# Optimization experiments

Hardware: AMD Instinct MI355X
Metric: run time of the kernel (lower is better)

Reference implementation:

```python
import jax, jax.numpy as jnp
import numpy as np

N_NET = 4000000   # length of concatenated model output values
R = 1000000       # number of rotated sp blocks (s0=9, s1=3)
NG = 1024         # number of geometries in the single bsize group
B = 64            # basis size (orbitals per molecule)
NE = 7            # number of elements for Eref
EREP = 2000000    # repulsive pair terms
ROT_LEN = 2 + R * 9


def setup_inputs() -> dict:
    key = jax.random.key(0)
    ks = jax.random.split(key, 14)
    net_vals = jax.random.normal(ks[0], (N_NET,), jnp.float32)
    rot_tensors = jax.random.normal(ks[1], (R, 9, 3), jnp.float32)
    S = jax.random.normal(ks[2], (NG, B, B), jnp.float32)
    S = 0.5 * (S + jnp.swapaxes(S, -2, -1))  # overlap is symmetric
    G = jax.random.normal(ks[3], (NG, B, B), jnp.float32)
    G = 0.5 * (G + jnp.swapaxes(G, -2, -1))  # gamma matrix is symmetric
    rho = jax.random.normal(ks[4], (NG, B, B), jnp.float32)
    qneutral = jax.random.uniform(ks[5], (NG, B, 1), dtype=jnp.float32)
    occ_rho_mask = (jax.random.uniform(ks[6], (NG, B, B)) > 0.5).astype(jnp.float32)
    phiS = 0.1 * jax.random.normal(ks[7], (NG, B, B), jnp.float32)
    zcounts = jax.random.uniform(ks[8], (1, NE), dtype=jnp.float32)
    ref_vars = jax.random.normal(ks[9], (NE,), jnp.float32)
    gather_rot = jax.random.randint(ks[10], (R * 3,), 0, N_NET)
    gather_oper = jax.random.randint(ks[11], (NG * B * B,), 0, ROT_LEN)
    gather_rep = jax.random.randint(ks[12], (EREP,), 0, N_NET)
    segsum_rep = jnp.sort(jax.random.randint(ks[13], (EREP,), 0, NG))
    return dict(net_vals=net_vals, rot_tensors=rot_tensors, S=S, G=G, rho=rho,
                qneutral=qneutral, occ_rho_mask=occ_rho_mask, phiS=phiS,
                zcounts=zcounts, ref_vars=ref_vars, gather_rot=gather_rot,
                gather_oper=gather_oper, gather_rep=gather_rep, segsum_rep=segsum_rep)


def reference(net_vals, rot_tensors, S, G, rho, qneutral, occ_rho_mask, phiS,
              zcounts, ref_vars, gather_rot, gather_oper, gather_rep, segsum_rep):
    ng, b, _ = S.shape
    # --- rotation stage: gather net_vals, batched small matmul [R,9,3]@[R,3,1]
    rot_vals = net_vals[gather_rot].reshape(-1, 3)[:, :, None]          # [R,3,1]
    rot = jnp.matmul(rot_tensors, rot_vals)[:, :, 0]                    # [R,9]
    rot_out = jnp.concatenate([jnp.array([0.0, 1.0], S.dtype), rot.reshape(-1)])
    # --- operator gather: build H blocks per geometry
    H = rot_out[gather_oper].reshape(ng, b, b)
    # --- charge fluctuations and coulomb matrix
    qbasis = rho * S
    dQ = qneutral - jnp.sum(qbasis, axis=2, keepdims=True)              # [ng,b,1]
    ep = jnp.matmul(G, dQ)                                              # [ng,b,1]
    couMat = -0.5 * S * (ep + jnp.swapaxes(ep, -2, -1))
    F = H + couMat
    # --- repulsive energy: gather + segment-sum over geometries
    Erep = jax.ops.segment_sum(net_vals[gather_rep], segsum_rep, num_segments=ng)
    # --- generalized eigenproblem via provided phiS (S^{-1/2})
    fockp = jnp.swapaxes(phiS, -2, -1) @ (F @ phiS)
    eorb, C = jnp.linalg.eigh(fockp)
    orb = phiS @ C
    orb_filled = occ_rho_mask * orb
    rho_out = 2.0 * (orb_filled @ jnp.swapaxes(orb_filled, -2, -1))
    # --- electronic energy
    ener1 = jnp.sum(rho_out * H, axis=(1, 2))
    ener2 = 0.5 * jnp.squeeze(jnp.swapaxes(dQ, -2, -1) @ (G @ dQ), axis=(1, 2))
    Eelec = ener1 + ener2
    Eref = jnp.dot(zcounts[0], ref_vars)
    return (H, dQ, Erep, eorb, rho_out, Eelec, Eref)
```

## Files before the change

### kernel.cpp

```cpp
#include <hip/hip_runtime.h>

typedef unsigned int uint_t;

#define NGc     1024
#define Bc      64
#define LDA     67
#define LDV     66
#define Rc      1000000
#define NNETc   4000000
#define EREPc   2000000
#define ROTLENc 9000002

#define OFF_H     0
#define OFF_DQ    4194304
#define OFF_EREP  4259840
#define OFF_EORB  4260864
#define OFF_RHO   4326400
#define OFF_EELEC 8520704
#define OFF_EREF  8521728

__global__ void k_rot(const float* __restrict__ rot_t,
                      const int*   __restrict__ gather_rot,
                      const float* __restrict__ net_vals,
                      float*       __restrict__ ws)
{
    int r = blockIdx.x * 256 + threadIdx.x;
    if (r >= Rc) return;
    const int* gr = gather_rot + (size_t)r * 3;
    int i0 = gr[0], i1 = gr[1], i2 = gr[2];
    i0 = ((unsigned)i0 < (unsigned)NNETc) ? i0 : 0;
    i1 = ((unsigned)i1 < (unsigned)NNETc) ? i1 : 0;
    i2 = ((unsigned)i2 < (unsigned)NNETc) ? i2 : 0;
    float v0 = net_vals[i0], v1 = net_vals[i1], v2 = net_vals[i2];
    const float* tt = rot_t + (size_t)r * 27;
    float* wp = ws + (size_t)r * 9;
    #pragma unroll
    for (int c = 0; c < 9; c++)
        wp[c] = tt[c*3+0] * v0 + tt[c*3+1] * v1 + tt[c*3+2] * v2;
}

__global__ void k_hgather4(const int*   __restrict__ idx,
                           const float* __restrict__ ws,
                           float*       __restrict__ out)
{
    int t4 = blockIdx.x * 256 + threadIdx.x;
    const int4 id4 = ((const int4*)idx)[t4];
    float4 hv;
    {
        int id = id4.x;
        hv.x = (id >= 2 && id < ROTLENc) ? ws[id - 2] : ((id == 1) ? 1.0f : 0.0f);
    }
    {
        int id = id4.y;
        hv.y = (id >= 2 && id < ROTLENc) ? ws[id - 2] : ((id == 1) ? 1.0f : 0.0f);
    }
    {
        int id = id4.z;
        hv.z = (id >= 2 && id < ROTLENc) ? ws[id - 2] : ((id == 1) ? 1.0f : 0.0f);
    }
    {
        int id = id4.w;
        hv.w = (id >= 2 && id < ROTLENc) ? ws[id - 2] : ((id == 1) ? 1.0f : 0.0f);
    }
    ((float4*)(out + OFF_H))[t4] = hv;
}

__global__ void k_hgather(const int*   __restrict__ idx,
                          const float* __restrict__ rot_t,
                          const int*   __restrict__ gather_rot,
                          const float* __restrict__ net_vals,
                          float*       __restrict__ out)
{
    int t = blockIdx.x * 256 + threadIdx.x;
    if (t >= NGc * Bc * Bc) return;
    int id = idx[t];
    float hv;
    if (id >= 2 && id < ROTLENc) {
        int k = id - 2;
        int r = k / 9;
        int c = k - r * 9;
        const float* tt = rot_t + (size_t)r * 27 + (size_t)c * 3;
        const int*   gr = gather_rot + (size_t)r * 3;
        int i0 = gr[0], i1 = gr[1], i2 = gr[2];
        i0 = ((unsigned)i0 < (unsigned)NNETc) ? i0 : 0;
        i1 = ((unsigned)i1 < (unsigned)NNETc) ? i1 : 0;
        i2 = ((unsigned)i2 < (unsigned)NNETc) ? i2 : 0;
        hv = tt[0] * net_vals[i0] + tt[1] * net_vals[i1] + tt[2] * net_vals[i2];
    } else {
        hv = (id == 1) ? 1.0f : 0.0f;
    }
    out[OFF_H + t] = hv;
}

__global__ void k_erep_seg(const float* __restrict__ net_vals,
                           const int*   __restrict__ gather_rep,
                           const int*   __restrict__ segsum,
                           const float* __restrict__ zcounts,
                           const float* __restrict__ ref_vars,
                           float*       __restrict__ out)
{
    __shared__ int   sB[2];
    __shared__ float red[256];
    const int g = blockIdx.x, tid = threadIdx.x;

    if (tid < 2) {
        int target = g + tid;
        int lo = 0, hi = EREPc;
        while (lo < hi) {
            int mid = (lo + hi) >> 1;
            if (segsum[mid] < target) lo = mid + 1; else hi = mid;
        }
        sB[tid] = lo;
    }
    __syncthreads();
    const int s = sB[0], e = sB[1];
    float acc = 0.f;
    for (int i = s + tid; i < e; i += 256) {
        int gi = gather_rep[i];
        gi = ((unsigned)gi < (unsigned)NNETc) ? gi : 0;
        acc += net_vals[gi];
    }
    red[tid] = acc;
    __syncthreads();
    for (int sN = 128; sN > 0; sN >>= 1) {
        if (tid < sN) red[tid] += red[tid + sN];
        __syncthreads();
    }
    if (tid == 0) out[OFF_EREP + g] = red[0];

    if (g == 0 && tid == 0) {
        float er = 0.f;
        for (int j = 0; j < 7; j++) er += zcounts[j] * ref_vars[j];
        out[OFF_EREF] = er;
    }
}

__global__ __launch_bounds__(256, 4) void k_geom(
    const float* __restrict__ Sg_,  const float* __restrict__ Gg_,
    const float* __restrict__ rho_, const float* __restrict__ qn_,
    const float* __restrict__ mask_,const float* __restrict__ phiS_,
    float* out)
{
    __shared__ float Ab[Bc * LDA];
    __shared__ float Vb[Bc * LDV];
    __shared__ float dqs[Bc];
    __shared__ float epv[Bc];
    __shared__ float red[256];
    __shared__ float diagA[Bc];
    __shared__ int   perm[Bc];
    __shared__ float2 csCS[32];
    __shared__ float sOffArr[4];

    const int g    = blockIdx.x;
    const int tid  = threadIdx.x;
    const size_t gb = (size_t)g * 4096;

    const float* Sp = Sg_  + gb;
    const float* Gp = Gg_  + gb;
    const float* Rp = rho_ + gb;
    const float* Mp = mask_+ gb;
    const float* Pp = phiS_+ gb;
    const float4* P4 = (const float4*)Pp;
    const float* Hp = out + OFF_H + gb;

    #pragma unroll
    for (int m = 0; m < 16; m++) {
        int e = tid + m * 256;
        int i = e >> 6, j = e & 63;
        Vb[i*LDV + j] = Sp[e];
    }
    __syncthreads();

    {
        int i = tid >> 2, qr = tid & 3;
        float acc = 0.f;
        #pragma unroll
        for (int jj = 0; jj < 16; jj++) {
            int j = qr * 16 + jj;
            acc += Rp[i * 64 + j] * Vb[i*LDV + j];
        }
        acc += __shfl_xor(acc, 1, 64);
        acc += __shfl_xor(acc, 2, 64);
        if (qr == 0) dqs[i] = qn_[(size_t)g * 64 + i] - acc;
    }
    #pragma unroll
    for (int m = 0; m < 16; m++) {
        int e = tid + m * 256;
        int i = e >> 6, j = e & 63;
        Ab[i*LDA + j] = Gp[e];
    }
    __syncthreads();
    {
        int i = tid >> 2, qr = tid & 3;
        float acc = 0.f;
        #pragma unroll
        for (int jj = 0; jj < 16; jj++) {
            int j = qr * 16 + jj;
            acc += Ab[i*LDA + j] * dqs[j];
        }
        acc += __shfl_xor(acc, 1, 64);
        acc += __shfl_xor(acc, 2, 64);
        if (qr == 0) epv[i] = acc;
    }
    __syncthreads();
    float ener2r = 0.f;
    if (tid < 64) {
        float v = dqs[tid] * epv[tid];
        #pragma unroll
        for (int o = 1; o < 64; o <<= 1) v += __shfl_xor(v, o, 64);
        if (tid == 0) ener2r = 0.5f * v;
    }
    #pragma unroll
    for (int m = 0; m < 16; m++) {
        int e = tid + m * 256;
        int i = e >> 6, j = e & 63;
        Ab[i*LDA + j] = Hp[e] - 0.5f * Vb[i*LDV + j] * (epv[i] + epv[j]);
    }
    __syncthreads();

    const int tx = tid & 15, ty = tid >> 4;
    const int row0 = ty * 4, col0 = tx * 4;
    float acc4[4][4];

    #pragma unroll
    for (int u = 0; u < 4; u++)
        #pragma unroll
        for (int v = 0; v < 4; v++) acc4[u][v] = 0.f;
    for (int k = 0; k < 64; k++) {
        float av[4];
        #pragma unroll
        for (int u = 0; u < 4; u++) av[u] = Ab[(row0 + u) * LDA + k];
        union { float4 v4; float f[4]; } b4;
        b4.v4 = P4[k * 16 + tx];
        #pragma unroll
        for (int u = 0; u < 4; u++)
            #pragma unroll
            for (int v = 0; v < 4; v++) acc4[u][v] += av[u] * b4.f[v];
    }
    #pragma unroll
    for (int u = 0; u < 4; u++)
        #pragma unroll
        for (int v = 0; v < 4; v++) Vb[(row0 + u) * LDV + col0 + v] = acc4[u][v];
    __syncthreads();

    #pragma unroll
    for (int u = 0; u < 4; u++)
        #pragma unroll
        for (int v = 0; v < 4; v++) acc4[u][v] = 0.f;
    for (int k = 0; k < 64; k++) {
        union { float4 v4; float f[4]; } a4;
        a4.v4 = P4[k * 16 + ty];
        float bv[4];
        #pragma unroll
        for (int v = 0; v < 4; v++) bv[v] = Vb[k * LDV + col0 + v];
        #pragma unroll
        for (int u = 0; u < 4; u++)
            #pragma unroll
            for (int v = 0; v < 4; v++) acc4[u][v] += a4.f[u] * bv[v];
    }
    {
        float fr = 0.f;
        #pragma unroll
        for (int u = 0; u < 4; u++)
            #pragma unroll
            for (int v = 0; v < 4; v++) {
                Ab[(row0 + u) * LDA + col0 + v] = acc4[u][v];
                fr += acc4[u][v] * acc4[u][v];
            }
        if (tx == ty) {
            #pragma unroll
            for (int u = 0; u < 4; u++) diagA[row0 + u] = acc4[u][u];
        }
        red[tid] = fr;
    }
    __syncthreads();
    for (int sN = 128; sN > 0; sN >>= 1) {
        if (tid < sN) red[tid] += red[tid + sN];
        __syncthreads();
    }
    const float anorm2 = red[0];

    #pragma unroll
    for (int m = 0; m < 17; m++) {
        int e = tid + m * 256;
        if (e < Bc * LDV) Vb[e] = 0.f;
    }
    __syncthreads();
    if (tid < 64) { Vb[tid * LDV + tid] = 1.f; perm[tid] = tid; }

    const float skip2 = anorm2 * 1e-18f;
    const float conv2 = anorm2 * 4e-14f;

    const int myi = tid & 31;
    const int jb  = tid >> 5;
    const int cb  = jb << 3;

    int iP, iQ, iPa, iQa, iPv, iQv;
    {
        iP = (myi == 0) ? 63 : myi;
        iQ = (myi == 0) ? 0  : 63 - myi;
        iPa = iP * LDA; iQa = iQ * LDA;
        iPv = iP * LDV; iQv = iQ * LDV;
    }
    int jP[4], jQ[4];
    #pragma unroll
    for (int k = 0; k < 4; k++) {
        int x = jb + (k << 3);
        jP[k] = (x == 0) ? 63 : x;
        jQ[k] = (x == 0) ? 0  : 63 - x;
    }
    const bool dgk[4] = { myi == jb, myi == jb + 8,
                          myi == jb + 16, myi == jb + 24 };

    for (int sweep = 0; sweep < 10; ++sweep) {
        float offacc = 0.f;
        for (int r = 0; r < 63; r++) {
            if (tid < 32) {
                float app = diagA[iP];
                float aqq = diagA[iQ];
                float apq = Ab[iPa + iQ];
                float a2 = apq * apq;
                offacc += a2;
                float c = 1.f, s = 0.f;
                if (a2 > skip2) {
                    float tau = (aqq - app) * __builtin_amdgcn_rcpf(apq + apq);
                    float tt = __builtin_amdgcn_rcpf(
                        fabsf(tau) + __builtin_amdgcn_sqrtf(1.f + tau * tau));
                    tt = (tau < 0.f) ? -tt : tt;
                    c = __builtin_amdgcn_rsqf(1.f + tt * tt);
                    s = tt * c;
                    diagA[iP] = app - tt * apq;
                    diagA[iQ] = aqq + tt * apq;
                    Ab[iPa + iQ] = 0.f;
                    Ab[iQa + iP] = 0.f;
                }
                csCS[myi] = make_float2(c, s);
            }
            __syncthreads();

            float2 me = csCS[myi];
            const float cO = me.x, sO = me.y;
            #pragma unroll
            for (int k = 0; k < 4; k++) {
                float2 cj = csCS[jb + (k << 3)];
                float cc = cj.x, ss = cj.y;
                if (!dgk[k] && (sO != 0.f || ss != 0.f)) {
                    int aPP = iPa + jP[k], aPQ = iPa + jQ[k];
                    int aQP = iQa + jP[k], aQQ = iQa + jQ[k];
                    float a = Ab[aPP], b = Ab[aPQ];
                    float d = Ab[aQP], e = Ab[aQQ];
                    float a1 = cc * a - ss * b, b1 = ss * a + cc * b;
                    float d1 = cc * d - ss * e, e1 = ss * d + cc * e;
                    Ab[aPP] = cO * a1 - sO * d1;
                    Ab[aQP] = sO * a1 + cO * d1;
                    Ab[aPQ] = cO * b1 - sO * e1;
                    Ab[aQQ] = sO * b1 + cO * e1;
                }
            }
            if (sO != 0.f) {
                float2* vp = (float2*)&Vb[iPv + cb];
                float2* vq = (float2*)&Vb[iQv + cb];
                #pragma unroll
                for (int e2 = 0; e2 < 4; e2++) {
                    float2 xp = vp[e2], xq = vq[e2];
                    float2 np, nq;
                    np.x = cO * xp.x - sO * xq.x;  np.y = cO * xp.y - sO * xq.y;
                    nq.x = sO * xp.x + cO * xq.x;  nq.y = sO * xp.y + cO * xq.y;
                    vp[e2] = np; vq[e2] = nq;
                }
            }
            {
                int nP  = (iP == 62) ? 0 : ((iP == 63) ? 63 : iP + 1);
                int nPa = (iP == 62) ? 0 : ((iP == 63) ? iPa : iPa + LDA);
                int nPv = (iP == 62) ? 0 : ((iP == 63) ? iPv : iPv + LDV);
                int nQ  = (iQ == 62) ? 0 : iQ + 1;
                int nQa = (iQ == 62) ? 0 : iQa + LDA;
                int nQv = (iQ == 62) ? 0 : iQv + LDV;
                iP = nP; iPa = nPa; iPv = nPv; iQ = nQ; iQa = nQa; iQv = nQv;
            }
            #pragma unroll
            for (int k = 0; k < 4; k++) {
                int p = jP[k], q = jQ[k];
                jP[k] = (p == 62) ? 0 : ((p == 63) ? 63 : p + 1);
                jQ[k] = (q == 62) ? 0 : q + 1;
            }
            __syncthreads();
        }
        float t2 = offacc;
        #pragma unroll
        for (int o = 1; o < 32; o <<= 1) t2 += __shfl_xor(t2, o, 64);
        if (tid == 0) sOffArr[0] = t2;
        __syncthreads();
        if (sOffArr[0] < conv2) break;
    }

    if (tid < 64) {
        float e = diagA[tid]; int rk = 0;
        for (int j = 0; j < 64; j++) {
            float ej = diagA[j];
            rk += (ej < e || (ej == e && j < tid)) ? 1 : 0;
        }
        rk &= 63;
        perm[rk] = tid;
        out[OFF_EORB + (size_t)g * 64 + rk] = e;
    }
    __syncthreads();

    {
        int pc0 = perm[col0 + 0] & 63, pc1 = perm[col0 + 1] & 63;
        int pc2 = perm[col0 + 2] & 63, pc3 = perm[col0 + 3] & 63;
        #pragma unroll
        for (int u = 0; u < 4; u++)
            #pragma unroll
            for (int v = 0; v < 4; v++) acc4[u][v] = 0.f;
        for (int kk = 0; kk < 16; kk++) {
            union { float4 v4; float f[4]; } a0, a1, a2u, a3;
            a0.v4  = P4[(row0 + 0) * 16 + kk];
            a1.v4  = P4[(row0 + 1) * 16 + kk];
            a2u.v4 = P4[(row0 + 2) * 16 + kk];
            a3.v4  = P4[(row0 + 3) * 16 + kk];
            #pragma unroll
            for (int t = 0; t < 4; t++) {
                int k = (kk << 2) + t;
                float b0 = Vb[pc0*LDV + k], b1 = Vb[pc1*LDV + k];
                float b2 = Vb[pc2*LDV + k], b3 = Vb[pc3*LDV + k];
                acc4[0][0] += a0.f[t]  * b0; acc4[0][1] += a0.f[t]  * b1;
                acc4[0][2] += a0.f[t]  * b2; acc4[0][3] += a0.f[t]  * b3;
                acc4[1][0] += a1.f[t]  * b0; acc4[1][1] += a1.f[t]  * b1;
                acc4[1][2] += a1.f[t]  * b2; acc4[1][3] += a1.f[t]  * b3;
                acc4[2][0] += a2u.f[t] * b0; acc4[2][1] += a2u.f[t] * b1;
                acc4[2][2] += a2u.f[t] * b2; acc4[2][3] += a2u.f[t] * b3;
                acc4[3][0] += a3.f[t]  * b0; acc4[3][1] += a3.f[t]  * b1;
                acc4[3][2] += a3.f[t]  * b2; acc4[3][3] += a3.f[t]  * b3;
            }
        }
        __syncthreads();
        #pragma unroll
        for (int u = 0; u < 4; u++)
            #pragma unroll
            for (int v = 0; v < 4; v++) Ab[(row0 + u) * LDA + col0 + v] = acc4[u][v];
    }
    __syncthreads();
    #pragma unroll
    for (int m = 0; m < 16; m++) {
        int e = tid + m * 256;
        int i = e >> 6, j = e & 63;
        Ab[i*LDA + j] *= Mp[e];
    }
    __syncthreads();

    #pragma unroll
    for (int u = 0; u < 4; u++)
        #pragma unroll
        for (int v = 0; v < 4; v++) acc4[u][v] = 0.f;
    for (int k = 0; k < 64; k++) {
        float av[4], bv[4];
        #pragma unroll
        for (int u = 0; u < 4; u++) av[u] = Ab[(row0 + u) * LDA + k];
        #pragma unroll
        for (int v = 0; v < 4; v++) bv[v] = Ab[(col0 + v) * LDA + k];
        #pragma unroll
        for (int u = 0; u < 4; u++)
            #pragma unroll
            for (int v = 0; v < 4; v++) acc4[u][v] += av[u] * bv[v];
    }
    {
        float e1 = 0.f;
        float* outR = out + OFF_RHO + gb;
        #pragma unroll
        for (int u = 0; u < 4; u++)
            #pragma unroll
            for (int v = 0; v < 4; v++) {
                float rv = 2.f * acc4[u][v];
                int i = row0 + u, j = col0 + v;
                outR[i * 64 + j] = rv;
                e1 += rv * Hp[i * 64 + j];
            }
        red[tid] = e1;
    }
    __syncthreads();
    for (int sN = 128; sN > 0; sN >>= 1) {
        if (tid < sN) red[tid] += red[tid + sN];
        __syncthreads();
    }
    if (tid == 0) out[OFF_EELEC + g] = red[0] + ener2r;
    if (tid < 64) out[OFF_DQ + (size_t)g * 64 + tid] = dqs[tid];
}

extern "C" void kernel_launch(void* const* d_in, const int* in_sizes, int n_in,
                              void* d_out, int out_size, void* d_ws, size_t ws_size,
                              hipStream_t stream)
{
    (void)in_sizes; (void)n_in; (void)out_size;
    const float* net_vals    = (const float*)d_in[0];
    const float* rot_tensors = (const float*)d_in[1];
    const float* S           = (const float*)d_in[2];
    const float* G           = (const float*)d_in[3];
    const float* rho         = (const float*)d_in[4];
    const float* qneutral    = (const float*)d_in[5];
    const float* mask        = (const float*)d_in[6];
    const float* phiS        = (const float*)d_in[7];
    const float* zcounts     = (const float*)d_in[8];
    const float* ref_vars    = (const float*)d_in[9];
    const int* gather_rot    = (const int*)d_in[10];
    const int* gather_oper   = (const int*)d_in[11];
    const int* gather_rep    = (const int*)d_in[12];
    const int* segsum_rep    = (const int*)d_in[13];

    float* out = (float*)d_out;

    const size_t need = (size_t)Rc * 9 * sizeof(float);
    if (d_ws && ws_size >= need) {
        k_rot<<<(Rc + 255) / 256, 256, 0, stream>>>(rot_tensors, gather_rot,
                                                    net_vals, (float*)d_ws);
        k_hgather4<<<4096, 256, 0, stream>>>(gather_oper, (const float*)d_ws, out);
    } else {
        k_hgather<<<16384, 256, 0, stream>>>(gather_oper, rot_tensors, gather_rot,
                                             net_vals, out);
    }
    k_erep_seg<<<NGc, 256, 0, stream>>>(net_vals, gather_rep, segsum_rep,
                                        zcounts, ref_vars, out);
    k_geom<<<NGc, 256, 0, stream>>>(S, G, rho, qneutral, mask, phiS, out);
}
```

Before: 1.388 ms.

## Exploit symmetry in Jacobi sweeps by updating only upper-triangle block pairs

The parallel Jacobi eigensolver now rotates only the 496 unordered off-diagonal 2x2 block pairs (i<j), not every ordered pair. Each thread owns at most two pairs, and every element is addressed through its upper-triangle location via min/max index mapping. This roughly halves LDS reads, writes and FMAs per rotation step. In exchange it adds index arithmetic, some threads do one pair and others two, and it assumes the lower triangle is never read afterwards.

New measurement: 1.300 ms. -6.3%, faster.

```diff
diff --git a/kernel.cpp b/kernel.cpp
--- a/kernel.cpp
+++ b/kernel.cpp
@@ -295,30 +295,38 @@
     const int jb  = tid >> 5;
     const int cb  = jb << 3;
 
-    int iP, iQ, iPa, iQa, iPv, iQv;
-    {
-        iP = (myi == 0) ? 63 : myi;
-        iQ = (myi == 0) ? 0  : 63 - myi;
-        iPa = iP * LDA; iQa = iQ * LDA;
-        iPv = iP * LDV; iQv = iQ * LDV;
-    }
-    int jP[4], jQ[4];
-    #pragma unroll
-    for (int k = 0; k < 4; k++) {
-        int x = jb + (k << 3);
-        jP[k] = (x == 0) ? 63 : x;
-        jQ[k] = (x == 0) ? 0  : 63 - x;
-    }
-    const bool dgk[4] = { myi == jb, myi == jb + 8,
-                          myi == jb + 16, myi == jb + 24 };
+    int myP = (myi == 0) ? 63 : myi;
+    int myQ = (myi == 0) ? 0  : 63 - myi;
+    int iPv = myP * LDV, iQv = myQ * LDV;
+
+    int bi1, bj1, bi2 = 0, bj2 = 1;
+    {
+        int m = tid, i = 0;
+        while (m >= 31 - i) { m -= 31 - i; ++i; }
+        bi1 = i; bj1 = i + 1 + m;
+    }
+    const bool hasB2 = (tid + 256) < 496;
+    if (hasB2) {
+        int m = tid + 256, i = 0;
+        while (m >= 31 - i) { m -= 31 - i; ++i; }
+        bi2 = i; bj2 = i + 1 + m;
+    }
+    int pI1 = (bi1 == 0) ? 63 : bi1, qI1 = (bi1 == 0) ? 0 : 63 - bi1;
+    int pJ1 = bj1,                   qJ1 = 63 - bj1;
+    int pI2 = (bi2 == 0) ? 63 : bi2, qI2 = (bi2 == 0) ? 0 : 63 - bi2;
+    int pJ2 = bj2,                   qJ2 = 63 - bj2;
+
+    #define ADVI(v) v = ((v) == 62) ? 0 : (((v) == 63) ? 63 : (v) + 1)
 
     for (int sweep = 0; sweep < 10; ++sweep) {
         float offacc = 0.f;
         for (int r = 0; r < 63; r++) {
             if (tid < 32) {
-                float app = diagA[iP];
-                float aqq = diagA[iQ];
-                float apq = Ab[iPa + iQ];
+                float app = diagA[myP];
+                float aqq = diagA[myQ];
+                int mn = min(myP, myQ), mx = max(myP, myQ);
+                int apqA = mn * LDA + mx;
+                float apq = Ab[apqA];
                 float a2 = apq * apq;
                 offacc += a2;
                 float c = 1.f, s = 0.f;
@@ -329,61 +337,69 @@
                     tt = (tau < 0.f) ? -tt : tt;
                     c = __builtin_amdgcn_rsqf(1.f + tt * tt);
                     s = tt * c;
-                    diagA[iP] = app - tt * apq;
-                    diagA[iQ] = aqq + tt * apq;
-                    Ab[iPa + iQ] = 0.f;
-                    Ab[iQa + iP] = 0.f;
+                    diagA[myP] = app - tt * apq;
+                    diagA[myQ] = aqq + tt * apq;
+                    Ab[apqA] = 0.f;
                 }
                 csCS[myi] = make_float2(c, s);
             }
             __syncthreads();
 
-            float2 me = csCS[myi];
-            const float cO = me.x, sO = me.y;
-            #pragma unroll
-            for (int k = 0; k < 4; k++) {
-                float2 cj = csCS[jb + (k << 3)];
-                float cc = cj.x, ss = cj.y;
-                if (!dgk[k] && (sO != 0.f || ss != 0.f)) {
-                    int aPP = iPa + jP[k], aPQ = iPa + jQ[k];
-                    int aQP = iQa + jP[k], aQQ = iQa + jQ[k];
-                    float a = Ab[aPP], b = Ab[aPQ];
-                    float d = Ab[aQP], e = Ab[aQQ];
-                    float a1 = cc * a - ss * b, b1 = ss * a + cc * b;
-                    float d1 = cc * d - ss * e, e1 = ss * d + cc * e;
-                    Ab[aPP] = cO * a1 - sO * d1;
-                    Ab[aQP] = sO * a1 + cO * d1;
-                    Ab[aPQ] = cO * b1 - sO * e1;
-                    Ab[aQQ] = sO * b1 + cO * e1;
+            {
+                float2 AI = csCS[bi1], AJ = csCS[bj1];
+                if (AI.y != 0.f || AJ.y != 0.f) {
+                    int mn, mx;
+                    mn = min(pI1,pJ1); mx = max(pI1,pJ1); int aA = mn*LDA + mx;
+                    mn = min(pI1,qJ1); mx = max(pI1,qJ1); int aB = mn*LDA + mx;
+                    mn = min(qI1,pJ1); mx = max(qI1,pJ1); int aD = mn*LDA + mx;
+                    mn = min(qI1,qJ1); mx = max(qI1,qJ1); int aE = mn*LDA + mx;
+                    float a = Ab[aA], b = Ab[aB], d = Ab[aD], e = Ab[aE];
+                    float a1 = AJ.x*a - AJ.y*b, b1 = AJ.y*a + AJ.x*b;
+                    float d1 = AJ.x*d - AJ.y*e, e1 = AJ.y*d + AJ.x*e;
+                    Ab[aA] = AI.x*a1 - AI.y*d1;
+                    Ab[aD] = AI.y*a1 + AI.x*d1;
+                    Ab[aB] = AI.x*b1 - AI.y*e1;
+                    Ab[aE] = AI.y*b1 + AI.x*e1;
                 }
             }
-            if (sO != 0.f) {
-                float2* vp = (float2*)&Vb[iPv + cb];
-                float2* vq = (float2*)&Vb[iQv + cb];
-                #pragma unroll
-                for (int e2 = 0; e2 < 4; e2++) {
-                    float2 xp = vp[e2], xq = vq[e2];
-                    float2 np, nq;
-                    np.x = cO * xp.x - sO * xq.x;  np.y = cO * xp.y - sO * xq.y;
-                    nq.x = sO * xp.x + cO * xq.x;  nq.y = sO * xp.y + cO * xq.y;
-                    vp[e2] = np; vq[e2] = nq;
+            if (hasB2) {
+                float2 AI = csCS[bi2], AJ = csCS[bj2];
+                if (AI.y != 0.f || AJ.y != 0.f) {
+                    int mn, mx;
+                    mn = min(pI2,pJ2); mx = max(pI2,pJ2); int aA = mn*LDA + mx;
+                    mn = min(pI2,qJ2); mx = max(pI2,qJ2); int aB = mn*LDA + mx;
+                    mn = min(qI2,pJ2); mx = max(qI2,pJ2); int aD = mn*LDA + mx;
+                    mn = min(qI2,qJ2); mx = max(qI2,qJ2); int aE = mn*LDA + mx;
+                    float a = Ab[aA], b = Ab[aB], d = Ab[aD], e = Ab[aE];
+                    float a1 = AJ.x*a - AJ.y*b, b1 = AJ.y*a + AJ.x*b;
+                    float d1 = AJ.x*d - AJ.y*e, e1 = AJ.y*d + AJ.x*e;
+                    Ab[aA] = AI.x*a1 - AI.y*d1;
+                    Ab[aD] = AI.y*a1 + AI.x*d1;
+                    Ab[aB] = AI.x*b1 - AI.y*e1;
+                    Ab[aE] = AI.y*b1 + AI.x*e1;
                 }
             }
             {
-                int nP  = (iP == 62) ? 0 : ((iP == 63) ? 63 : iP + 1);
-                int nPa = (iP == 62) ? 0 : ((iP == 63) ? iPa : iPa + LDA);
-                int nPv = (iP == 62) ? 0 : ((iP == 63) ? iPv : iPv + LDV);
-                int nQ  = (iQ == 62) ? 0 : iQ + 1;
-                int nQa = (iQ == 62) ? 0 : iQa + LDA;
-                int nQv = (iQ == 62) ? 0 : iQv + LDV;
-                iP = nP; iPa = nPa; iPv = nPv; iQ = nQ; iQa = nQa; iQv = nQv;
-            }
-            #pragma unroll
-            for (int k = 0; k < 4; k++) {
-                int p = jP[k], q = jQ[k];
-                jP[k] = (p == 62) ? 0 : ((p == 63) ? 63 : p + 1);
-                jQ[k] = (q == 62) ? 0 : q + 1;
-            }
+                float2 me = csCS[myi];
+                if (me.y != 0.f) {
+                    const float cO = me.x, sO = me.y;
+                    float2* vp = (float2*)&Vb[iPv + cb];
+                    float2* vq = (float2*)&Vb[iQv + cb];
+                    #pragma unroll
+                    for (int e2 = 0; e2 < 4; e2++) {
+                        float2 xp = vp[e2], xq = vq[e2];
+                        float2 np, nq;
+                        np.x = cO * xp.x - sO * xq.x;  np.y = cO * xp.y - sO * xq.y;
+                        nq.x = sO * xp.x + cO * xq.x;  nq.y = sO * xp.y + cO * xq.y;
+                        vp[e2] = np; vq[e2] = nq;
+                    }
+                }
+            }
+            iPv = (myP == 62) ? 0 : ((myP == 63) ? iPv : iPv + LDV);
+            iQv = (myQ == 62) ? 0 : iQv + LDV;
+            ADVI(myP); ADVI(myQ);
+            ADVI(pI1); ADVI(qI1); ADVI(pJ1); ADVI(qJ1);
+            ADVI(pI2); ADVI(qI2); ADVI(pJ2); ADVI(qJ2);
             __syncthreads();
         }
         float t2 = offacc;
@@ -393,6 +409,7 @@
         __syncthreads();
         if (sOffArr[0] < conv2) break;
     }
+    #undef ADVI
 
     if (tid < 64) {
         float e = diagA[tid]; int rk = 0;
```
